# Performance work log

Measured on AMD Instinct MI355X. Metric: run time of the kernel, lower is better.

## Reference

```python
import jax, jax.numpy as jnp
import numpy as np

B, S, D_MODEL, N_HEADS, HEAD_DIM = 4, 2048, 1024, 16, 64
NEG = -1e9


def apply_rope_real(x, cos_f, sin_f):
    # x: [B, H, S, D]; cos_f/sin_f: [S, D//2] broadcast over B, H
    x_even = x[..., ::2]
    x_odd = x[..., 1::2]
    out_even = x_even * cos_f - x_odd * sin_f
    out_odd = x_even * sin_f + x_odd * cos_f
    return jnp.stack([out_even, out_odd], axis=-1).reshape(x.shape)


def setup_inputs() -> dict:
    key = jax.random.key(0)
    ks = jax.random.split(key, 8)
    x = jax.random.normal(ks[0], (B, S, D_MODEL), dtype=jnp.float32)
    # RoPE tables: theta_i = 10000^{-2i/d}, angles = pos * theta
    inv_freq = 1.0 / (10000.0 ** (jnp.arange(0, HEAD_DIM, 2, dtype=jnp.float32) / HEAD_DIM))
    angles = jnp.arange(S, dtype=jnp.float32)[:, None] * inv_freq[None, :]  # [S, D/2]
    cos_freqs = jnp.cos(angles)
    sin_freqs = jnp.sin(angles)
    causal_mask = jnp.where(jnp.tril(jnp.ones((S, S), dtype=bool)), 0.0, NEG).astype(jnp.float32)
    scale = 0.02
    w_q = jax.random.normal(ks[1], (D_MODEL, D_MODEL), dtype=jnp.float32) * scale
    w_k = jax.random.normal(ks[2], (D_MODEL, D_MODEL), dtype=jnp.float32) * scale
    w_v = jax.random.normal(ks[3], (D_MODEL, D_MODEL), dtype=jnp.float32) * scale
    w_o = jax.random.normal(ks[4], (D_MODEL, D_MODEL), dtype=jnp.float32) * scale
    return {"x": x, "cos_freqs": cos_freqs, "sin_freqs": sin_freqs,
            "causal_mask": causal_mask, "w_q": w_q, "w_k": w_k, "w_v": w_v, "w_o": w_o}


def reference(x, cos_freqs, sin_freqs, causal_mask, w_q, w_k, w_v, w_o):
    batch, seq_len, _ = x.shape
    scale = 1.0 / jnp.sqrt(jnp.float32(HEAD_DIM))
    # torch Linear: y = x @ W.T
    def proj(w):
        return (x @ w.T).reshape(batch, seq_len, N_HEADS, HEAD_DIM).transpose(0, 2, 1, 3)
    q = apply_rope_real(proj(w_q), cos_freqs, sin_freqs)
    k = apply_rope_real(proj(w_k), cos_freqs, sin_freqs)
    v = proj(w_v)
    attn = jnp.einsum('bhqd,bhkd->bhqk', q, k) * scale + causal_mask
    attn = jax.nn.softmax(attn, axis=-1)
    out = jnp.einsum('bhqk,bhkd->bhqd', attn, v)
    out = out.transpose(0, 2, 1, 3).reshape(batch, seq_len, -1)
    return out @ w_o.T
```

## Files before the change

### kernel.cpp

```cpp
#include <hip/hip_runtime.h>
#include <stdint.h>

#define B_  4
#define S_  2048
#define DM_ 1024
#define NH_ 16
#define HD_ 64

typedef unsigned short ushort_t;
typedef __bf16 bf16x8 __attribute__((ext_vector_type(8)));
typedef float  floatx4 __attribute__((ext_vector_type(4)));
typedef float  floatx16 __attribute__((ext_vector_type(16)));

__device__ __forceinline__ float bf2f(ushort_t u) {
    union { unsigned int i; float f; } v; v.i = ((unsigned int)u) << 16; return v.f;
}
__device__ __forceinline__ ushort_t f2bf(float f) {
    union { float f; unsigned int i; } v; v.f = f;
    unsigned int x = v.i;
    return (ushort_t)((x + 0x7fffu + ((x >> 16) & 1u)) >> 16);
}
__device__ __forceinline__ unsigned int pack_bf16_trunc(float lo, float hi) {
    union { float f; unsigned int u; } a, b;
    a.f = lo; b.f = hi;
    return __builtin_amdgcn_perm(b.u, a.u, 0x07060302u);
}

__global__ __launch_bounds__(256) void cvt_kernel(
    const float* __restrict__ src, ushort_t* __restrict__ dst)
{
    const int i = blockIdx.x * 256 + threadIdx.x;
    float4 v = ((const float4*)src)[i];
    ushort4 o; o.x = f2bf(v.x); o.y = f2bf(v.y); o.z = f2bf(v.z); o.w = f2bf(v.w);
    ((ushort4*)dst)[i] = o;
}

__global__ __launch_bounds__(256) void cvt4_kernel(
    const float* __restrict__ s0, const float* __restrict__ s1,
    const float* __restrict__ s2, const float* __restrict__ s3,
    ushort_t* __restrict__ d0, ushort_t* __restrict__ d1,
    ushort_t* __restrict__ d2, ushort_t* __restrict__ d3)
{
    const int z = blockIdx.y;
    const float* s = z == 0 ? s0 : z == 1 ? s1 : z == 2 ? s2 : s3;
    ushort_t*   d = z == 0 ? d0 : z == 1 ? d1 : z == 2 ? d2 : d3;
    const int i = blockIdx.x * 256 + threadIdx.x;
    float4 v = ((const float4*)s)[i];
    ushort4 o; o.x = f2bf(v.x); o.y = f2bf(v.y); o.z = f2bf(v.z); o.w = f2bf(v.w);
    ((ushort4*)d)[i] = o;
}

__global__ __launch_bounds__(256) void gemm_bt_kernel(
    const ushort_t* __restrict__ A,
    const ushort_t* __restrict__ B0, const ushort_t* __restrict__ B1,
    const ushort_t* __restrict__ B2,
    void* __restrict__ C0, void* __restrict__ C1, void* __restrict__ C2,
    int M, int N, int K, int mode)
{
    __shared__ ushort_t As[128 * 32];
    __shared__ ushort_t Bs[128 * 32];
    const int z = blockIdx.z;
    const ushort_t* Bw = z == 0 ? B0 : z == 1 ? B1 : B2;
    void* Cv           = z == 0 ? C0 : z == 1 ? C1 : C2;

    const int tid  = threadIdx.x;
    const int mbase = blockIdx.x * 128;
    const int nbase = blockIdx.y * 128;
    const int wave = tid >> 6, lane = tid & 63;
    const int l15 = lane & 15, quad = lane >> 4;
    const int wm = (wave & 1) * 64, wn = (wave >> 1) * 64;

    floatx4 acc[4][4] = {};

    const int e0   = tid * 8;
    const int row0 = e0 >> 5;
    const int col0 = e0 & 31;

    for (int kt = 0; kt < K; kt += 32) {
        __syncthreads();
#pragma unroll
        for (int r = 0; r < 2; ++r) {
            const int e   = e0 + r * 2048;
            const int row = row0 + r * 64;
            const ushort_t* ga = A  + (size_t)(mbase + row) * K + kt + col0;
            const ushort_t* gb = Bw + (size_t)(nbase + row) * K + kt + col0;
            __builtin_amdgcn_global_load_lds(
                (const __attribute__((address_space(1))) unsigned int*)ga,
                (__attribute__((address_space(3))) unsigned int*)(As + e), 16, 0, 0);
            __builtin_amdgcn_global_load_lds(
                (const __attribute__((address_space(1))) unsigned int*)gb,
                (__attribute__((address_space(3))) unsigned int*)(Bs + e), 16, 0, 0);
        }
        __builtin_amdgcn_s_waitcnt(0);
        __syncthreads();

        bf16x8 af[4], bfr[4];
#pragma unroll
        for (int t = 0; t < 4; ++t) {
            af[t]  = *(const bf16x8*)(As + (wm + t * 16 + l15) * 32 + quad * 8);
            bfr[t] = *(const bf16x8*)(Bs + (wn + t * 16 + l15) * 32 + quad * 8);
        }
#pragma unroll
        for (int mt = 0; mt < 4; ++mt)
#pragma unroll
            for (int nt = 0; nt < 4; ++nt)
                acc[mt][nt] = __builtin_amdgcn_mfma_f32_16x16x32_bf16(
                    af[mt], bfr[nt], acc[mt][nt], 0, 0, 0);
    }

#pragma unroll
    for (int mt = 0; mt < 4; ++mt) {
#pragma unroll
        for (int nt = 0; nt < 4; ++nt) {
            const int col = nbase + wn + nt * 16 + l15;
#pragma unroll
            for (int r = 0; r < 4; ++r) {
                const int m = mbase + wm + mt * 16 + quad * 4 + r;
                if (mode == 0) {
                    const int b = m >> 11, s = m & 2047;
                    const int hh = col >> 6, d = col & 63;
                    ((ushort_t*)Cv)[(((size_t)(b * NH_ + hh)) * S_ + s) * HD_ + d] =
                        f2bf(acc[mt][nt][r]);
                } else {
                    ((float*)Cv)[(size_t)m * N + col] = acc[mt][nt][r];
                }
            }
        }
    }
}

__global__ __launch_bounds__(256) void rope_kernel(
    ushort_t* __restrict__ q, ushort_t* __restrict__ k,
    const float* __restrict__ cf, const float* __restrict__ sf)
{
    const int idx = blockIdx.x * 256 + threadIdx.x;
    const int j = idx & 31;
    const int s = (idx >> 5) & (S_ - 1);
    const float c  = cf[s * 32 + j];
    const float sn = sf[s * 32 + j];
    const size_t base = (size_t)idx * 2;
    float qe = bf2f(q[base]), qo = bf2f(q[base + 1]);
    q[base]     = f2bf((qe * c - qo * sn) * 0.125f);
    q[base + 1] = f2bf((qe * sn + qo * c) * 0.125f);
    float ke = bf2f(k[base]), ko = bf2f(k[base + 1]);
    k[base]     = f2bf(ke * c - ko * sn);
    k[base + 1] = f2bf(ke * sn + ko * c);
}

__global__ __launch_bounds__(256, 2) void attn_kernel(
    const ushort_t* __restrict__ Qg, const ushort_t* __restrict__ Kg,
    const ushort_t* __restrict__ Vg, ushort_t* __restrict__ Og)
{
    __shared__ ushort_t Ks[64 * 72];
    __shared__ ushort_t Vt[64 * 72];
    __shared__ ushort_t Pt[4][32 * 72];

    const int pair = blockIdx.x;
    const int bh   = blockIdx.y;
    const int tid  = threadIdx.x;
    const int wave = tid >> 6, lane = tid & 63;
    const int l31 = lane & 31, h = lane >> 5;

    const size_t bh_off = (size_t)bh * S_ * HD_;
    const int trow = tid >> 3;
    const int tcol = (tid & 7) * 8;
    const int vswz = (tid & 7) << 3;
    const int b_out = bh >> 4, h_out = bh & 15;

#pragma unroll 1
    for (int seg = 0; seg < 2; ++seg) {
        const int qtile = seg ? (15 - pair) : pair;
        const int qbase = qtile * 128;
        const int nkt   = 2 * qtile + 2;
        const int qrow  = qbase + wave * 32 + l31;

        bf16x8 qf[4];
#pragma unroll
        for (int ks = 0; ks < 4; ++ks)
            qf[ks] = *(const bf16x8*)(Qg + bh_off + (size_t)qrow * HD_ + ks * 16 + h * 8);

        float m_run = -1e30f, l_run = 0.f;
        floatx16 o_acc[2] = {};

        for (int kt = 0; kt < nkt; ++kt) {
            const int kbase = kt * 64;
            __syncthreads();
#pragma unroll
            for (int r = 0; r < 2; ++r) {
                const int row = trow + r * 32;
                *(bf16x8*)(Ks + row * 72 + tcol) =
                    *(const bf16x8*)(Kg + bh_off + (size_t)(kbase + row) * HD_ + tcol);
                union { bf16x8 v; ushort_t u[8]; } vv;
                vv.v = *(const bf16x8*)(Vg + bh_off + (size_t)(kbase + row) * HD_ + tcol);
#pragma unroll
                for (int i = 0; i < 8; ++i)
                    Vt[(tcol + i) * 72 + (row ^ vswz)] = vv.u[i];
            }
            __syncthreads();

            if (kbase > qbase + wave * 32 + 31) continue;

            floatx16 st[2] = {};
#pragma unroll
            for (int nt = 0; nt < 2; ++nt) {
                const ushort_t* kr = Ks + (nt * 32 + l31) * 72 + h * 8;
#pragma unroll
                for (int ks = 0; ks < 4; ++ks) {
                    bf16x8 kf = *(const bf16x8*)(kr + ks * 16);
                    st[nt] = __builtin_amdgcn_mfma_f32_32x32x16_bf16(kf, qf[ks], st[nt], 0, 0, 0);
                }
            }
            if (kbase + 63 > qbase + wave * 32) {
#pragma unroll
                for (int nt = 0; nt < 2; ++nt) {
                    const int key0 = kbase + nt * 32 + 4 * h;
#pragma unroll
                    for (int c = 0; c < 4; ++c)
#pragma unroll
                        for (int r = 0; r < 4; ++r)
                            if (key0 + 8 * c + r > qrow) st[nt][c * 4 + r] = -1e9f;
                }
            }
            float mx = st[0][0];
#pragma unroll
            for (int nt = 0; nt < 2; ++nt)
#pragma unroll
                for (int i = 0; i < 16; ++i) mx = fmaxf(mx, st[nt][i]);
            mx = fmaxf(mx, __shfl_xor(mx, 32, 64));
            const float mnew = fmaxf(m_run, mx);
            const float alpha = __expf(m_run - mnew);
            m_run = mnew;
            float sum = 0.f;
#pragma unroll
            for (int nt = 0; nt < 2; ++nt)
#pragma unroll
                for (int i = 0; i < 16; ++i) {
                    const float p = __expf(st[nt][i] - mnew);
                    st[nt][i] = p; sum += p;
                }
            sum += __shfl_xor(sum, 32, 64);
            l_run = l_run * alpha + sum;
#pragma unroll
            for (int dt = 0; dt < 2; ++dt)
#pragma unroll
                for (int i = 0; i < 16; ++i) o_acc[dt][i] *= alpha;

            ushort_t* pr = &Pt[wave][l31 * 72 + 4 * h];
#pragma unroll
            for (int nt = 0; nt < 2; ++nt)
#pragma unroll
                for (int c = 0; c < 4; ++c) {
                    uint2 pk;
                    pk.x = pack_bf16_trunc(st[nt][c * 4 + 0], st[nt][c * 4 + 1]);
                    pk.y = pack_bf16_trunc(st[nt][c * 4 + 2], st[nt][c * 4 + 3]);
                    *(uint2*)(pr + nt * 32 + 8 * c) = pk;
                }
            __builtin_amdgcn_fence(__ATOMIC_ACQ_REL, "wavefront");
            __builtin_amdgcn_wave_barrier();

            bf16x8 pf[4];
#pragma unroll
            for (int ks = 0; ks < 4; ++ks)
                pf[ks] = *(const bf16x8*)(&Pt[wave][l31 * 72 + ks * 16 + h * 8]);

#pragma unroll
            for (int dt = 0; dt < 2; ++dt) {
                const int d = dt * 32 + l31;
                const int sw = ((d >> 3) & 7) << 3;
                const ushort_t* vr = Vt + d * 72;
#pragma unroll
                for (int ks = 0; ks < 4; ++ks) {
                    bf16x8 vf = *(const bf16x8*)(vr + ((ks * 16 + h * 8) ^ sw));
                    o_acc[dt] = __builtin_amdgcn_mfma_f32_32x32x16_bf16(vf, pf[ks], o_acc[dt], 0, 0, 0);
                }
            }
        }

        const float inv = 1.0f / l_run;
        ushort_t* orow = Og + ((size_t)(b_out * S_ + qrow)) * DM_ + h_out * HD_;
#pragma unroll
        for (int dt = 0; dt < 2; ++dt)
#pragma unroll
            for (int c = 0; c < 4; ++c) {
                uint2 pk;
                pk.x = (unsigned)f2bf(o_acc[dt][c * 4 + 0] * inv) |
                       ((unsigned)f2bf(o_acc[dt][c * 4 + 1] * inv) << 16);
                pk.y = (unsigned)f2bf(o_acc[dt][c * 4 + 2] * inv) |
                       ((unsigned)f2bf(o_acc[dt][c * 4 + 3] * inv) << 16);
                *(uint2*)(orow + dt * 32 + 8 * c + 4 * h) = pk;
            }
    }
}

extern "C" void kernel_launch(void* const* d_in, const int* in_sizes, int n_in,
                              void* d_out, int out_size, void* d_ws, size_t ws_size,
                              hipStream_t stream)
{
    const float* x  = (const float*)d_in[0];
    const float* cf = (const float*)d_in[1];
    const float* sf = (const float*)d_in[2];
    const float* wq = (const float*)d_in[4];
    const float* wk = (const float*)d_in[5];
    const float* wv = (const float*)d_in[6];
    const float* wo = (const float*)d_in[7];
    float* out = (float*)d_out;

    const size_t NELEM = (size_t)B_ * S_ * DM_;
    const size_t WELEM = (size_t)DM_ * DM_;
    ushort_t* xb  = (ushort_t*)d_ws;
    ushort_t* qb  = xb + NELEM;
    ushort_t* kb  = qb + NELEM;
    ushort_t* vb  = kb + NELEM;
    ushort_t* ao  = vb + NELEM;
    ushort_t* wqb = ao + NELEM;
    ushort_t* wkb = wqb + WELEM;
    ushort_t* wvb = wkb + WELEM;
    ushort_t* wob = wvb + WELEM;

    cvt_kernel<<<dim3(NELEM / 1024), 256, 0, stream>>>(x, xb);
    cvt4_kernel<<<dim3(WELEM / 1024, 4), 256, 0, stream>>>(
        wq, wk, wv, wo, wqb, wkb, wvb, wob);

    const int M = B_ * S_;
    gemm_bt_kernel<<<dim3(M / 128, DM_ / 128, 3), 256, 0, stream>>>(
        xb, wqb, wkb, wvb, qb, kb, vb, M, DM_, DM_, 0);
    rope_kernel<<<dim3((B_ * NH_ * S_ * 32) / 256), 256, 0, stream>>>(qb, kb, cf, sf);
    attn_kernel<<<dim3(8, B_ * NH_), 256, 0, stream>>>(qb, kb, vb, ao);
    gemm_bt_kernel<<<dim3(M / 128, DM_ / 128, 1), 256, 0, stream>>>(
        ao, wob, wob, wob, out, out, out, M, DM_, DM_, 1);
}
```

Before: 303.0 us.

## Fuse conversions, deepen GEMM K-tile, pre-transpose V, exp2 softmax, swizzle P

Folds the activation and weight bf16 conversions into one launch, and doubles the GEMM K-step to 64 so there are half as many barriers per tile. The QKV GEMM now writes V pre-transposed (head-dim-major), which lets attention load V with vector stores instead of a scalar transpose. The log2(e) factor moves into the Q scale so softmax can use the native exp2 instruction. The P staging buffer drops its padding in favour of an XOR swizzle. The risks are higher LDS use in the GEMM and the scattered 8-byte stores needed for the V-transposed epilogue.

```diff
diff --git a/kernel.cpp b/kernel.cpp
--- a/kernel.cpp
+++ b/kernel.cpp
@@ -26,28 +26,25 @@
     return __builtin_amdgcn_perm(b.u, a.u, 0x07060302u);
 }
 
-__global__ __launch_bounds__(256) void cvt_kernel(
-    const float* __restrict__ src, ushort_t* __restrict__ dst)
-{
-    const int i = blockIdx.x * 256 + threadIdx.x;
+__global__ __launch_bounds__(256) void cvt_all_kernel(
+    const float* __restrict__ x,  const float* __restrict__ wq,
+    const float* __restrict__ wk, const float* __restrict__ wv,
+    const float* __restrict__ wo,
+    ushort_t* __restrict__ xb,  ushort_t* __restrict__ wqb,
+    ushort_t* __restrict__ wkb, ushort_t* __restrict__ wvb,
+    ushort_t* __restrict__ wob)
+{
+    const int blk = blockIdx.x;
+    const float* src; ushort_t* dst; int off;
+    if (blk < 8192)       { src = x;  dst = xb;  off = blk; }
+    else if (blk < 9216)  { src = wq; dst = wqb; off = blk - 8192; }
+    else if (blk < 10240) { src = wk; dst = wkb; off = blk - 9216; }
+    else if (blk < 11264) { src = wv; dst = wvb; off = blk - 10240; }
+    else                  { src = wo; dst = wob; off = blk - 11264; }
+    const int i = off * 256 + threadIdx.x;
     float4 v = ((const float4*)src)[i];
     ushort4 o; o.x = f2bf(v.x); o.y = f2bf(v.y); o.z = f2bf(v.z); o.w = f2bf(v.w);
     ((ushort4*)dst)[i] = o;
-}
-
-__global__ __launch_bounds__(256) void cvt4_kernel(
-    const float* __restrict__ s0, const float* __restrict__ s1,
-    const float* __restrict__ s2, const float* __restrict__ s3,
-    ushort_t* __restrict__ d0, ushort_t* __restrict__ d1,
-    ushort_t* __restrict__ d2, ushort_t* __restrict__ d3)
-{
-    const int z = blockIdx.y;
-    const float* s = z == 0 ? s0 : z == 1 ? s1 : z == 2 ? s2 : s3;
-    ushort_t*   d = z == 0 ? d0 : z == 1 ? d1 : z == 2 ? d2 : d3;
-    const int i = blockIdx.x * 256 + threadIdx.x;
-    float4 v = ((const float4*)s)[i];
-    ushort4 o; o.x = f2bf(v.x); o.y = f2bf(v.y); o.z = f2bf(v.z); o.w = f2bf(v.w);
-    ((ushort4*)d)[i] = o;
 }
 
 __global__ __launch_bounds__(256) void gemm_bt_kernel(
@@ -57,8 +54,8 @@
     void* __restrict__ C0, void* __restrict__ C1, void* __restrict__ C2,
     int M, int N, int K, int mode)
 {
-    __shared__ ushort_t As[128 * 32];
-    __shared__ ushort_t Bs[128 * 32];
+    __shared__ ushort_t As[128 * 64];
+    __shared__ ushort_t Bs[128 * 64];
     const int z = blockIdx.z;
     const ushort_t* Bw = z == 0 ? B0 : z == 1 ? B1 : B2;
     void* Cv           = z == 0 ? C0 : z == 1 ? C1 : C2;
@@ -72,18 +69,16 @@
 
     floatx4 acc[4][4] = {};
 
-    const int e0   = tid * 8;
-    const int row0 = e0 >> 5;
-    const int col0 = e0 & 31;
-
-    for (int kt = 0; kt < K; kt += 32) {
+    for (int kt = 0; kt < K; kt += 64) {
         __syncthreads();
 #pragma unroll
-        for (int r = 0; r < 2; ++r) {
-            const int e   = e0 + r * 2048;
-            const int row = row0 + r * 64;
-            const ushort_t* ga = A  + (size_t)(mbase + row) * K + kt + col0;
-            const ushort_t* gb = Bw + (size_t)(nbase + row) * K + kt + col0;
+        for (int r = 0; r < 4; ++r) {
+            const int e   = tid * 8 + r * 2048;
+            const int kk  = e >> 12;
+            const int row = (e >> 5) & 127;
+            const int c   = e & 31;
+            const ushort_t* ga = A  + (size_t)(mbase + row) * K + kt + kk * 32 + c;
+            const ushort_t* gb = Bw + (size_t)(nbase + row) * K + kt + kk * 32 + c;
             __builtin_amdgcn_global_load_lds(
                 (const __attribute__((address_space(1))) unsigned int*)ga,
                 (__attribute__((address_space(3))) unsigned int*)(As + e), 16, 0, 0);
@@ -94,41 +89,56 @@
         __builtin_amdgcn_s_waitcnt(0);
         __syncthreads();
 
-        bf16x8 af[4], bfr[4];
-#pragma unroll
-        for (int t = 0; t < 4; ++t) {
-            af[t]  = *(const bf16x8*)(As + (wm + t * 16 + l15) * 32 + quad * 8);
-            bfr[t] = *(const bf16x8*)(Bs + (wn + t * 16 + l15) * 32 + quad * 8);
+#pragma unroll
+        for (int kk = 0; kk < 2; ++kk) {
+            bf16x8 af[4], bfr[4];
+#pragma unroll
+            for (int t = 0; t < 4; ++t) {
+                af[t]  = *(const bf16x8*)(As + kk * 4096 + (wm + t * 16 + l15) * 32 + quad * 8);
+                bfr[t] = *(const bf16x8*)(Bs + kk * 4096 + (wn + t * 16 + l15) * 32 + quad * 8);
+            }
+#pragma unroll
+            for (int mt = 0; mt < 4; ++mt)
+#pragma unroll
+                for (int nt = 0; nt < 4; ++nt)
+                    acc[mt][nt] = __builtin_amdgcn_mfma_f32_16x16x32_bf16(
+                        af[mt], bfr[nt], acc[mt][nt], 0, 0, 0);
         }
-#pragma unroll
-        for (int mt = 0; mt < 4; ++mt)
-#pragma unroll
-            for (int nt = 0; nt < 4; ++nt)
-                acc[mt][nt] = __builtin_amdgcn_mfma_f32_16x16x32_bf16(
-                    af[mt], bfr[nt], acc[mt][nt], 0, 0, 0);
     }
 
+    const bool vtmode = (mode == 0) && (z == 2);
 #pragma unroll
     for (int mt = 0; mt < 4; ++mt) {
 #pragma unroll
         for (int nt = 0; nt < 4; ++nt) {
             const int col = nbase + wn + nt * 16 + l15;
-#pragma unroll
-            for (int r = 0; r < 4; ++r) {
-                const int m = mbase + wm + mt * 16 + quad * 4 + r;
-                if (mode == 0) {
+            const int m0  = mbase + wm + mt * 16 + quad * 4;
+            if (vtmode) {
+                const int b = m0 >> 11, s = m0 & 2047;
+                const int hh = col >> 6, d = col & 63;
+                uint2 pk;
+                pk.x = (unsigned)f2bf(acc[mt][nt][0]) | ((unsigned)f2bf(acc[mt][nt][1]) << 16);
+                pk.y = (unsigned)f2bf(acc[mt][nt][2]) | ((unsigned)f2bf(acc[mt][nt][3]) << 16);
+                *(uint2*)&((ushort_t*)Cv)[((size_t)((b * NH_ + hh) * HD_ + d)) * S_ + s] = pk;
+            } else if (mode == 0) {
+#pragma unroll
+                for (int r = 0; r < 4; ++r) {
+                    const int m = m0 + r;
                     const int b = m >> 11, s = m & 2047;
                     const int hh = col >> 6, d = col & 63;
                     ((ushort_t*)Cv)[(((size_t)(b * NH_ + hh)) * S_ + s) * HD_ + d] =
                         f2bf(acc[mt][nt][r]);
-                } else {
-                    ((float*)Cv)[(size_t)m * N + col] = acc[mt][nt][r];
-                }
+                }
+            } else {
+#pragma unroll
+                for (int r = 0; r < 4; ++r)
+                    ((float*)Cv)[(size_t)(m0 + r) * N + col] = acc[mt][nt][r];
             }
         }
     }
 }
 
+#define QSCALE 0.1803368801f
 __global__ __launch_bounds__(256) void rope_kernel(
     ushort_t* __restrict__ q, ushort_t* __restrict__ k,
     const float* __restrict__ cf, const float* __restrict__ sf)
@@ -140,8 +150,8 @@
     const float sn = sf[s * 32 + j];
     const size_t base = (size_t)idx * 2;
     float qe = bf2f(q[base]), qo = bf2f(q[base + 1]);
-    q[base]     = f2bf((qe * c - qo * sn) * 0.125f);
-    q[base + 1] = f2bf((qe * sn + qo * c) * 0.125f);
+    q[base]     = f2bf((qe * c - qo * sn) * QSCALE);
+    q[base + 1] = f2bf((qe * sn + qo * c) * QSCALE);
     float ke = bf2f(k[base]), ko = bf2f(k[base + 1]);
     k[base]     = f2bf(ke * c - ko * sn);
     k[base + 1] = f2bf(ke * sn + ko * c);
@@ -153,7 +163,7 @@
 {
     __shared__ ushort_t Ks[64 * 72];
     __shared__ ushort_t Vt[64 * 72];
-    __shared__ ushort_t Pt[4][32 * 72];
+    __shared__ ushort_t Pt[4][32 * 64];
 
     const int pair = blockIdx.x;
     const int bh   = blockIdx.y;
@@ -164,7 +174,7 @@
     const size_t bh_off = (size_t)bh * S_ * HD_;
     const int trow = tid >> 3;
     const int tcol = (tid & 7) * 8;
-    const int vswz = (tid & 7) << 3;
+    const int pswz = (l31 & 7) << 3;
     const int b_out = bh >> 4, h_out = bh & 15;
 
 #pragma unroll 1
@@ -190,11 +200,10 @@
                 const int row = trow + r * 32;
                 *(bf16x8*)(Ks + row * 72 + tcol) =
                     *(const bf16x8*)(Kg + bh_off + (size_t)(kbase + row) * HD_ + tcol);
-                union { bf16x8 v; ushort_t u[8]; } vv;
-                vv.v = *(const bf16x8*)(Vg + bh_off + (size_t)(kbase + row) * HD_ + tcol);
-#pragma unroll
-                for (int i = 0; i < 8; ++i)
-                    Vt[(tcol + i) * 72 + (row ^ vswz)] = vv.u[i];
+                const int c = tid + r * 256;
+                const int d = c >> 3, k0 = (c & 7) * 8;
+                bf16x8 vv = *(const bf16x8*)(Vg + bh_off + (size_t)d * S_ + kbase + k0);
+                *(bf16x8*)(Vt + d * 72 + (k0 ^ (((d >> 3) & 7) << 3))) = vv;
             }
             __syncthreads();
 
@@ -228,14 +237,14 @@
                 for (int i = 0; i < 16; ++i) mx = fmaxf(mx, st[nt][i]);
             mx = fmaxf(mx, __shfl_xor(mx, 32, 64));
             const float mnew = fmaxf(m_run, mx);
-            const float alpha = __expf(m_run - mnew);
+            const float alpha = __builtin_amdgcn_exp2f(m_run - mnew);
             m_run = mnew;
             float sum = 0.f;
 #pragma unroll
             for (int nt = 0; nt < 2; ++nt)
 #pragma unroll
                 for (int i = 0; i < 16; ++i) {
-                    const float p = __expf(st[nt][i] - mnew);
+                    const float p = __builtin_amdgcn_exp2f(st[nt][i] - mnew);
                     st[nt][i] = p; sum += p;
                 }
             sum += __shfl_xor(sum, 32, 64);
@@ -245,7 +254,7 @@
 #pragma unroll
                 for (int i = 0; i < 16; ++i) o_acc[dt][i] *= alpha;
 
-            ushort_t* pr = &Pt[wave][l31 * 72 + 4 * h];
+            ushort_t* pr = &Pt[wave][l31 * 64];
 #pragma unroll
             for (int nt = 0; nt < 2; ++nt)
 #pragma unroll
@@ -253,7 +262,7 @@
                     uint2 pk;
                     pk.x = pack_bf16_trunc(st[nt][c * 4 + 0], st[nt][c * 4 + 1]);
                     pk.y = pack_bf16_trunc(st[nt][c * 4 + 2], st[nt][c * 4 + 3]);
-                    *(uint2*)(pr + nt * 32 + 8 * c) = pk;
+                    *(uint2*)(pr + (((nt * 32 + 8 * c) ^ pswz) + 4 * h)) = pk;
                 }
             __builtin_amdgcn_fence(__ATOMIC_ACQ_REL, "wavefront");
             __builtin_amdgcn_wave_barrier();
@@ -261,7 +270,7 @@
             bf16x8 pf[4];
 #pragma unroll
             for (int ks = 0; ks < 4; ++ks)
-                pf[ks] = *(const bf16x8*)(&Pt[wave][l31 * 72 + ks * 16 + h * 8]);
+                pf[ks] = *(const bf16x8*)(&Pt[wave][l31 * 64 + ((ks * 16 + h * 8) ^ pswz)]);
 
 #pragma unroll
             for (int dt = 0; dt < 2; ++dt) {
@@ -317,9 +326,8 @@
     ushort_t* wvb = wkb + WELEM;
     ushort_t* wob = wvb + WELEM;
 
-    cvt_kernel<<<dim3(NELEM / 1024), 256, 0, stream>>>(x, xb);
-    cvt4_kernel<<<dim3(WELEM / 1024, 4), 256, 0, stream>>>(
-        wq, wk, wv, wo, wqb, wkb, wvb, wob);
+    cvt_all_kernel<<<dim3(8192 + 4 * 1024), 256, 0, stream>>>(
+        x, wq, wk, wv, wo, xb, wqb, wkb, wvb, wob);
 
     const int M = B_ * S_;
     gemm_bt_kernel<<<dim3(M / 128, DM_ / 128, 3), 256, 0, stream>>>(
```

Result: faster. 285.8 us (-5.7%).
